# Kernel tuning notes

Measured on AMD Instinct MI355X. Metric: run time of the kernel, lower is better.

The kernel has to match this reference:

```python
import jax, jax.numpy as jnp
import numpy as np
from jax import lax

B, S, D = 8, 96, 768
R, RSEQ, TAG = 24, 8, 3


def setup_inputs() -> dict:
    key = jax.random.key(0)
    k0, k1, k2, k3 = jax.random.split(key, 4)
    encoded_text = jax.random.normal(k0, (B, S, D), jnp.float32)
    rel_types_encoded = jax.random.normal(k1, (R, RSEQ, D), jnp.float32)
    proj_W = jax.random.normal(k2, (2 * D, 3 * D), jnp.float32) * 0.02
    proj_b = jnp.zeros((3 * D,), jnp.float32)
    rel_W = jax.random.normal(k3, (3 * D, R * TAG), jnp.float32) * 0.02
    rel_b = jnp.zeros((R * TAG,), jnp.float32)
    return {
        "encoded_text": encoded_text,
        "rel_types_encoded": rel_types_encoded,
        "proj_W": proj_W,
        "proj_b": proj_b,
        "rel_W": rel_W,
        "rel_b": rel_b,
    }


def _refine(enc, rel_types):
    """Faithful vectorized version of the nested python loops in
    get_encoded_text: for each sample i, R sequential cross-attention
    updates on matrix_b using matrix_a = rel_types_encoded[i] (the
    original code indexes with i, reusing the same matrix_a each step).
    enc: [Bsz, S, D]; rel_types: [R, RSEQ, D].
    """
    Bsz = enc.shape[0]
    d = enc.shape[-1]
    scale = 1.0 / jnp.sqrt(jnp.asarray(d, enc.dtype))
    num_steps = rel_types.shape[0]  # loop runs rel_types_encoded.size(0) times
    A_batch = rel_types[:Bsz]  # matrix_a = rel_types_encoded[i]

    def per_sample(b0, A):  # b0: [S, D], A: [RSEQ, D]
        def step(b, _):
            scores = (A @ b.T) * scale            # [RSEQ, S]
            w = jax.nn.softmax(scores, axis=-1)    # softmax over seq
            return b + w.T @ A, None               # matrix_b += matrix_c
        bf, _ = lax.scan(step, b0, None, length=num_steps)
        return bf

    return jax.vmap(per_sample)(enc, A_batch)


def reference(encoded_text, rel_types_encoded, proj_W, proj_b, rel_W, rel_b):
    enc = _refine(encoded_text, rel_types_encoded)  # [B, S, D]
    Bsz, seq, d = enc.shape
    rel_num = rel_types_encoded.shape[0]
    tag_size = rel_W.shape[1] // rel_num

    # projection(cat(head, tail)) == head @ Wh + tail @ Wt + b; avoid
    # materializing the [B, S*S, 2D] concat (same math as the original).
    Wh, Wt = proj_W[:d], proj_W[d:]
    Hh = enc @ Wh                                   # [B, S, 3D] head part
    Ht = enc @ Wt                                   # [B, S, 3D] tail part
    pairs = Hh[:, :, None, :] + Ht[:, None, :, :] + proj_b  # [B, S, S, 3D]
    pairs = jax.nn.relu(pairs)
    triple = pairs.reshape(Bsz, seq * seq, 3 * d) @ rel_W + rel_b
    triple = triple.reshape(Bsz, seq, seq, rel_num, tag_size)
    return jnp.transpose(triple, (0, 4, 3, 1, 2))  # [B, tag, rel, S, S]
```

## Files before the change

### kernel.cpp

```cpp
#include <hip/hip_runtime.h>
#include <hip/hip_bf16.h>
#include <math.h>
#include <stdint.h>
#include <string.h>

#define BB 8
#define SS 96
#define DD 768
#define RR 24
#define RSEQ 8
#define TAG 3
#define D3 2304
#define NC 72

typedef __attribute__((ext_vector_type(8))) short bf16x8;
typedef __attribute__((ext_vector_type(4))) float f32x4;
typedef _Float16 f16x8 __attribute__((ext_vector_type(8)));
typedef _Float16 f16x2 __attribute__((ext_vector_type(2)));

typedef __attribute__((address_space(3))) uint8_t lds_u8;
typedef const __attribute__((address_space(1))) uint8_t glb_u8;
static __device__ __forceinline__ void glld16(const void* g, void* l) {
  __builtin_amdgcn_global_load_lds((glb_u8*)g, (lds_u8*)l, 16, 0, 0);
}

#define VMW(N) asm volatile("s_waitcnt vmcnt(" #N ")" ::: "memory")

static __device__ inline uint32_t pkrhu(float lo, float hi) {
  uint32_t a, b;
  memcpy(&a, &lo, 4);
  memcpy(&b, &hi, 4);
  return __builtin_amdgcn_perm(b + 0x8000u, a + 0x8000u, 0x07060302u);
}
static __device__ inline uint32_t pkrne(float lo, float hi) {
  uint32_t a, b;
  memcpy(&a, &lo, 4);
  memcpy(&b, &hi, 4);
  a += 0x7FFFu + ((a >> 16) & 1u);
  b += 0x7FFFu + ((b >> 16) & 1u);
  return (a >> 16) | (b & 0xFFFF0000u);
}
static __device__ inline uint32_t pkf16(float lo, float hi) {
  union { f16x2 h; uint32_t u; } r;
  r.h[0] = (_Float16)lo;
  r.h[1] = (_Float16)hi;
  return r.u;
}
static __device__ inline uint16_t f16b(float v) {
  union { _Float16 h; uint16_t u; } r;
  r.h = (_Float16)v;
  return r.u;
}

__global__ __launch_bounds__(256) void k_prep0(const float* __restrict__ relW,
                                               uint16_t* __restrict__ Wb,
                                               const float* __restrict__ projW,
                                               uint16_t* __restrict__ Tp,
                                               const float* __restrict__ enc,
                                               const float* __restrict__ rel,
                                               float* __restrict__ SG) {
  __shared__ __align__(16) char smem[24704];
  const int blk = blockIdx.x;
  const int t = threadIdx.x;

  if (blk < 36) {
    float* tile = (float*)smem;
    const int k0 = blk * 64;
    const float* src = relW + (size_t)k0 * NC;
    for (int e = t; e < 64 * NC / 4; e += 256) ((float4*)tile)[e] = ((const float4*)src)[e];
    __syncthreads();
    for (int u = t; u < 80 * 16; u += 256) {
      const int n = u >> 4, kq = (u & 15) * 4;
      uint2 w = {0u, 0u};
      if (n < NC) {
        w.x = pkf16(tile[(kq + 0) * NC + n], tile[(kq + 1) * NC + n]);
        w.y = pkf16(tile[(kq + 2) * NC + n], tile[(kq + 3) * NC + n]);
      }
      *(uint2*)&Wb[(size_t)n * D3 + k0 + kq] = w;
    }
  } else if (blk < 900) {
    const int bx = blk - 36;
    float (*tile)[65] = (float(*)[65])smem;
    const int c0 = (bx % 36) * 64;
    const int r0 = (bx / 36) * 64;
    {
      const int tr = t >> 4;
      const int tc4 = (t & 15) * 4;
#pragma unroll
      for (int p = 0; p < 4; ++p) {
        const int r = tr + p * 16;
        const float4 v = *(const float4*)&projW[(size_t)(r0 + r) * D3 + c0 + tc4];
        tile[r][tc4 + 0] = v.x;
        tile[r][tc4 + 1] = v.y;
        tile[r][tc4 + 2] = v.z;
        tile[r][tc4 + 3] = v.w;
      }
    }
    __syncthreads();
    {
      const int cc = t >> 4;
      const int rr4 = (t & 15) * 4;
#pragma unroll
      for (int p = 0; p < 4; ++p) {
        const int c = cc + p * 16;
        uint2 w;
        w.x = pkrne(tile[rr4 + 0][c], tile[rr4 + 1][c]);
        w.y = pkrne(tile[rr4 + 2][c], tile[rr4 + 3][c]);
        *(uint2*)&Tp[(size_t)(c0 + c) * (2 * DD) + r0 + rr4] = w;
      }
    }
  } else {
    const int idx = blk - 900;
    const int b = idx >> 4;
    const int d0 = (idx & 15) * 48;
    float (*AsF)[48] = (float(*)[48])smem;

    if (t < 96) {
      const int r = t / 12, q4 = (t % 12) * 4;
      *(float4*)&AsF[r][q4] = *(const float4*)&rel[((size_t)b * RSEQ + r) * DD + d0 + q4];
    }
    __syncthreads();

    for (int e = t; e < RSEQ * (SS + RSEQ); e += 256) {
      const int r = e & 7, s = e >> 3;
      const float* row = (s < SS) ? (enc + ((size_t)b * SS + s) * DD + d0) : &AsF[s - SS][0];
      float a0 = 0.f, a1 = 0.f, a2 = 0.f, a3 = 0.f;
#pragma unroll
      for (int d = 0; d < 48; d += 4) {
        const float4 rv = *(const float4*)&row[d];
        a0 += AsF[r][d + 0] * rv.x;
        a1 += AsF[r][d + 1] * rv.y;
        a2 += AsF[r][d + 2] * rv.z;
        a3 += AsF[r][d + 3] * rv.w;
      }
      atomicAdd(&SG[((size_t)b * RSEQ + r) * 104 + s], (a0 + a1) + (a2 + a3));
    }
  }
}

__global__ __launch_bounds__(256) void k_refS(const float* __restrict__ SG,
                                              float* __restrict__ Pst) {
  const int b = blockIdx.x;
  const int t = threadIdx.x;
  __shared__ float S0[RSEQ][SS];
  __shared__ float G[RSEQ][RSEQ];
  __shared__ float P[RSEQ][SS];
  __shared__ float sc[RSEQ][SS];
  const float scale = 0.036084391824351613f;

  for (int e = t; e < RSEQ * 104; e += 256) {
    const int r = e / 104, c = e % 104;
    const float v = SG[(size_t)b * RSEQ * 104 + e];
    if (c < SS) S0[r][c] = v;
    else G[r][c - SS] = v;
  }
  for (int e = t; e < RSEQ * SS; e += 256) ((float*)P)[e] = 0.f;
  __syncthreads();

  const int wave = t >> 6, lane = t & 63;
  for (int step = 0; step < RR; ++step) {
    for (int e = t; e < RSEQ * SS; e += 256) {
      const int r = e / SS, s = e % SS;
      float acc = S0[r][s];
#pragma unroll
      for (int r2 = 0; r2 < RSEQ; ++r2) acc += G[r][r2] * P[r2][s];
      sc[r][s] = acc * scale;
    }
    __syncthreads();
#pragma unroll
    for (int rr = 0; rr < 2; ++rr) {
      const int r = wave * 2 + rr;
      const float m1 = sc[r][lane];
      const float m2 = (lane < 32) ? sc[r][lane + 64] : -1e30f;
      float mx = fmaxf(m1, m2);
#pragma unroll
      for (int o = 32; o > 0; o >>= 1) mx = fmaxf(mx, __shfl_xor(mx, o, 64));
      const float e1 = __expf(m1 - mx);
      const float e2 = (lane < 32) ? __expf(m2 - mx) : 0.f;
      float sm = e1 + e2;
#pragma unroll
      for (int o = 32; o > 0; o >>= 1) sm += __shfl_xor(sm, o, 64);
      const float inv = 1.f / sm;
      P[r][lane] += e1 * inv;
      if (lane < 32) P[r][lane + 64] += e2 * inv;
    }
    __syncthreads();
  }

  for (int e = t; e < RSEQ * SS; e += 256) Pst[(size_t)b * RSEQ * SS + e] = ((float*)P)[e];
}

__global__ __launch_bounds__(256) void k_refB(const float* __restrict__ enc,
                                              const float* __restrict__ rel,
                                              const float* __restrict__ Pst,
                                              uint16_t* __restrict__ encRb) {
  const int blk = blockIdx.x;
  const int b = blk / 12;
  const int s0 = (blk % 12) * 8;
  const int t = threadIdx.x;
  __shared__ float As[RSEQ][DD + 4];
  __shared__ float Pl[RSEQ][8];

  const float* Ag = rel + (size_t)b * RSEQ * DD;
  for (int e = t; e < RSEQ * DD / 4; e += 256) {
    const int r = (e * 4) / DD, d = (e * 4) % DD;
    *(float4*)&As[r][d] = *(const float4*)&Ag[e * 4];
  }
  if (t < RSEQ * 8) {
    const int r = t >> 3, sl = t & 7;
    Pl[r][sl] = Pst[(size_t)b * RSEQ * SS + r * SS + s0 + sl];
  }
  __syncthreads();

  const float* Eb = enc + ((size_t)b * SS + s0) * DD;
  uint16_t* Ob = encRb + ((size_t)b * SS + s0) * DD;
  for (int e = t; e < 8 * DD / 4; e += 256) {
    const int sl = (e * 4) / DD, d = (e * 4) % DD;
    float4 v = ((const float4*)Eb)[e];
#pragma unroll
    for (int r = 0; r < RSEQ; ++r) {
      const float p = Pl[r][sl];
      v.x += p * As[r][d + 0];
      v.y += p * As[r][d + 1];
      v.z += p * As[r][d + 2];
      v.w += p * As[r][d + 3];
    }
    uint2 w;
    w.x = pkrhu(v.x, v.y);
    w.y = pkrhu(v.z, v.w);
    *(uint2*)&Ob[e * 4] = w;
  }
}

__global__ __launch_bounds__(256, 4) void k_proj(const uint16_t* __restrict__ Ab,
                                                 const uint16_t* __restrict__ Bt,
                                                 const float* __restrict__ pb,
                                                 uint16_t* __restrict__ Hh16,
                                                 uint16_t* __restrict__ Htf) {
  const int m0 = blockIdx.x * 64;
  const int gn0 = blockIdx.y * 64;
  const bool isH = gn0 < D3;
  const int n0 = isH ? gn0 : gn0 - D3;
  const int halfk = isH ? 0 : DD;
  const int t = threadIdx.x, w = t >> 6, lane = t & 63;
  const int wm = w >> 1, wn = w & 1;
  const int lm = lane & 15, q = lane >> 4;

  __shared__ __align__(16) uint16_t As[64 * 72];
  __shared__ __align__(16) uint16_t Bs[64 * 72];

  const char* rp[5];
  char* lp[5];
#pragma unroll
  for (int r = 0; r < 5; ++r) {
    const int idx = w + 4 * r;
    rp[r] = nullptr;
    lp[r] = nullptr;
    if (idx < 18) {
      const int ii = (idx < 9) ? idx : idx - 9;
      const int beta = ii * 1024 + lane * 16;
      const int elem = beta >> 1;
      const int row = elem / 72;
      int o = elem - row * 72;
      if (o >= 64) o = 0;
      if (idx < 9) {
        rp[r] = (const char*)(Ab + (size_t)(m0 + row) * DD + o);
        lp[r] = (char*)As + ii * 1024;
      } else {
        rp[r] = (const char*)(Bt + (size_t)(n0 + row) * (2 * DD) + halfk + o);
        lp[r] = (char*)Bs + ii * 1024;
      }
    }
  }

  f32x4 acc[2][2];
#pragma unroll
  for (int a = 0; a < 2; ++a)
#pragma unroll
    for (int c = 0; c < 2; ++c) acc[a][c] = (f32x4){0.f, 0.f, 0.f, 0.f};

  for (int k0 = 0; k0 < DD; k0 += 64) {
    __syncthreads();
#pragma unroll
    for (int r = 0; r < 5; ++r)
      if (rp[r]) glld16(rp[r] + 2 * k0, lp[r]);
    __syncthreads();
#pragma unroll
    for (int kk = 0; kk < 2; ++kk) {
      const int ko = kk * 32 + q * 8;
      bf16x8 af[2], bf[2];
#pragma unroll
      for (int mt = 0; mt < 2; ++mt)
        af[mt] = *(const bf16x8*)&As[(wm * 32 + mt * 16 + lm) * 72 + ko];
#pragma unroll
      for (int nt = 0; nt < 2; ++nt)
        bf[nt] = *(const bf16x8*)&Bs[(wn * 32 + nt * 16 + lm) * 72 + ko];
#pragma unroll
      for (int nt = 0; nt < 2; ++nt)
#pragma unroll
        for (int mt = 0; mt < 2; ++mt)
          acc[mt][nt] = __builtin_amdgcn_mfma_f32_16x16x32_bf16(af[mt], bf[nt], acc[mt][nt], 0, 0, 0);
    }
  }

#pragma unroll
  for (int nt = 0; nt < 2; ++nt) {
    const int ncol = n0 + wn * 32 + nt * 16 + lm;
    const int mrow = m0 + wm * 32 + q * 4;
    uint16_t* dst = isH ? Hh16 : Htf;
    const float bias = isH ? pb[ncol] : 0.f;
#pragma unroll
    for (int mt = 0; mt < 2; ++mt)
#pragma unroll
      for (int r = 0; r < 4; ++r)
        dst[(size_t)(mrow + mt * 16 + r) * D3 + ncol] = f16b(acc[mt][nt][r] + bias);
  }
}

#define HT_LDS 12288
#define CH_B 22528
#define NISS 22
#define NKC 36
#define NPH 18

__global__ __launch_bounds__(768, 1) void k_pairs(const uint16_t* __restrict__ Hh,
                                                  const uint16_t* __restrict__ Htb,
                                                  const uint16_t* __restrict__ Wb,
                                                  const float* __restrict__ relb,
                                                  float* __restrict__ out) {
  const int blk = blockIdx.x;
  const int b = blk >> 5, ii = blk & 31;
  const int t = threadIdx.x;
  const int w = t >> 6, lane = t & 63;
  const int lm = lane & 15, q = lane >> 4;
  const int iw = w >> 2;
  const int jh = (w >> 1) & 1;
  const int kh = w & 1;
  const int i = ii * 3 + iw;

  __shared__ __align__(16) uint16_t Hr[7680];
  __shared__ __align__(16) uint16_t Stg[3][CH_B];

  {
    const char* hh = (const char*)(Hh + ((size_t)b * SS + ii * 3) * D3);
#pragma unroll
    for (int r = 0; r < 2; ++r) {
      const int idx = w + 12 * r;
      if (idx < 14) glld16(hh + idx * 1024 + lane * 16, (char*)Hr + idx * 1024);
    }
  }

  const char* rp[2];
#pragma unroll
  for (int r = 0; r < 2; ++r) {
    const int idx = w + 12 * r;
    rp[r] = nullptr;
    if (idx < NISS) {
      const int beta = idx * 1024 + lane * 16;
      if (beta < HT_LDS) {
        const int row = beta >> 7;
        const int real = (beta & 127) ^ ((row & 7) << 4);
        rp[r] = (const char*)(Htb + ((size_t)b * SS + row) * D3 + (real >> 1));
      } else {
        const int bb = beta - HT_LDS;
        const int row = bb >> 7;
        const int real = (bb & 127) ^ ((row & 7) << 4);
        rp[r] = (const char*)(Wb + (size_t)row * D3 + (real >> 1));
      }
    }
  }

#pragma unroll
  for (int pp = 0; pp < 2; ++pp)
#pragma unroll
    for (int kc = 0; kc < 2; ++kc)
#pragma unroll
      for (int r = 0; r < 2; ++r)
        if (rp[r])
          glld16(rp[r] + (size_t)128 * (2 * pp + kc),
                 (char*)Stg[pp] + kc * CH_B + (w + 12 * r) * 1024);

  f32x4 acc[3][5];
#pragma unroll
  for (int mt = 0; mt < 3; ++mt)
#pragma unroll
    for (int nt = 0; nt < 5; ++nt) acc[mt][nt] = (f32x4){0.f, 0.f, 0.f, 0.f};

  const f16x8 zro = {0, 0, 0, 0, 0, 0, 0, 0};

  for (int p = 0; p < NPH; ++p) {
    if (w < 10) VMW(4); else VMW(2);
    __builtin_amdgcn_s_barrier();
    __builtin_amdgcn_sched_barrier(0);

    {
      char* dst = (char*)Stg[(p + 2) % 3];
      int pn = p + 2;
      if (pn >= NPH) pn -= NPH;
#pragma unroll
      for (int kc = 0; kc < 2; ++kc)
#pragma unroll
        for (int r = 0; r < 2; ++r)
          if (rp[r])
            glld16(rp[r] + (size_t)128 * (2 * pn + kc),
                   dst + kc * CH_B + (w + 12 * r) * 1024);
    }

    const char* S = (const char*)Stg[p % 3] + kh * CH_B;
    const int k0 = (2 * p + kh) * 64;
#pragma unroll
    for (int kk = 0; kk < 2; ++kk) {
      const int ko = kk * 32 + q * 8;
      const int xb = (ko * 2) ^ ((lane & 7) << 4);
      const f16x8 hv = *(const f16x8*)&Hr[iw * D3 + k0 + ko];
      f16x8 af[3];
#pragma unroll
      for (int mt = 0; mt < 3; ++mt) {
        const f16x8 s = *(const f16x8*)(S + (jh * 48 + mt * 16 + lm) * 128 + xb) + hv;
        af[mt] = __builtin_elementwise_max(s, zro);
      }
      f16x8 bfv[5];
#pragma unroll
      for (int nt = 0; nt < 5; ++nt)
        bfv[nt] = *(const f16x8*)(S + HT_LDS + (nt * 16 + lm) * 128 + xb);
      __builtin_amdgcn_s_setprio(1);
#pragma unroll
      for (int nt = 0; nt < 5; ++nt)
#pragma unroll
        for (int mt = 0; mt < 3; ++mt)
          acc[mt][nt] = __builtin_amdgcn_mfma_f32_16x16x32_f16(af[mt], bfv[nt], acc[mt][nt], 0, 0, 0);
      __builtin_amdgcn_s_setprio(0);
    }
    asm volatile("s_waitcnt lgkmcnt(0)" ::: "memory");
    __builtin_amdgcn_sched_barrier(0);
  }

  __syncthreads();
  float* RED = (float*)&Stg[0][0];
  if (w & 1) {
#pragma unroll
    for (int mt = 0; mt < 3; ++mt)
#pragma unroll
      for (int nt = 0; nt < 5; ++nt)
        *(f32x4*)&RED[(((w >> 1) * 15 + mt * 5 + nt) << 8) + lane * 4] = acc[mt][nt];
  }
  __syncthreads();
  if (!(w & 1)) {
#pragma unroll
    for (int nt = 0; nt < 5; ++nt) {
      const int c = nt * 16 + lm;
      if (c < NC) {
        const float rb = relb[c];
        const int rr = c / 3, tg = c % 3;
#pragma unroll
        for (int mt = 0; mt < 3; ++mt) {
          const f32x4 oth = *(const f32x4*)&RED[(((w >> 1) * 15 + mt * 5 + nt) << 8) + lane * 4];
          const int j0 = jh * 48 + mt * 16 + q * 4;
          float* base = out + ((((size_t)b * TAG + tg) * RR + rr) * SS + i) * SS + j0;
          float4 o;
          o.x = acc[mt][nt][0] + oth[0] + rb;
          o.y = acc[mt][nt][1] + oth[1] + rb;
          o.z = acc[mt][nt][2] + oth[2] + rb;
          o.w = acc[mt][nt][3] + oth[3] + rb;
          *(float4*)base = o;
        }
      }
    }
  }
}

extern "C" void kernel_launch(void* const* d_in, const int* in_sizes, int n_in,
                              void* d_out, int out_size, void* d_ws, size_t ws_size,
                              hipStream_t stream) {
  const float* enc   = (const float*)d_in[0];
  const float* rel   = (const float*)d_in[1];
  const float* projW = (const float*)d_in[2];
  const float* projb = (const float*)d_in[3];
  const float* relW  = (const float*)d_in[4];
  const float* relb  = (const float*)d_in[5];
  float* out = (float*)d_out;

  uint16_t* Hh16 = (uint16_t*)d_ws;
  uint16_t* Htf  = Hh16 + (size_t)DD * D3 + 512;
  uint16_t* Wb   = Htf + (size_t)DD * D3;
  uint16_t* Tp   = Wb + (size_t)96 * D3;
  uint16_t* Ab   = Tp + (size_t)D3 * 2 * DD;
  float* Pst = (float*)(Ab + (size_t)DD * DD);
  float* SG = Pst + (size_t)BB * RSEQ * SS;

  hipMemsetAsync(SG, 0, (size_t)BB * RSEQ * 104 * sizeof(float), stream);
  k_prep0<<<1028, 256, 0, stream>>>(relW, Wb, projW, Tp, enc, rel, SG);
  k_refS<<<BB, 256, 0, stream>>>(SG, Pst);
  k_refB<<<96, 256, 0, stream>>>(enc, rel, Pst, Ab);
  k_proj<<<dim3(12, 72), 256, 0, stream>>>(Ab, Tp, projb, Hh16, Htf);
  k_pairs<<<256, 768, 0, stream>>>(Hh16, Htf, Wb, relb, out);
}
```

Baseline: 182.1 us.

## Run refinement softmax in one register-resident wave; enlarge projection GEMM M tile

The 24-step softmax refinement now runs in a single 64-lane wave per sample. Scores, G and P live in registers, which removes the per-step LDS traffic and block barriers. Separately, the projection GEMM's M tile grows from 64 to 128 rows, so each block loads the B tile once for twice as many rows and the grid halves. The trade-offs are higher register pressure in both kernels and fewer blocks (432) to fill the GPU in k_proj.

```diff
diff --git a/kernel.cpp b/kernel.cpp
--- a/kernel.cpp
+++ b/kernel.cpp
@@ -138,56 +138,65 @@
   }
 }
 
-__global__ __launch_bounds__(256) void k_refS(const float* __restrict__ SG,
-                                              float* __restrict__ Pst) {
+__global__ __launch_bounds__(64) void k_refS(const float* __restrict__ SG,
+                                             float* __restrict__ Pst) {
   const int b = blockIdx.x;
-  const int t = threadIdx.x;
-  __shared__ float S0[RSEQ][SS];
-  __shared__ float G[RSEQ][RSEQ];
-  __shared__ float P[RSEQ][SS];
-  __shared__ float sc[RSEQ][SS];
+  const int l = threadIdx.x;
   const float scale = 0.036084391824351613f;
-
-  for (int e = t; e < RSEQ * 104; e += 256) {
-    const int r = e / 104, c = e % 104;
-    const float v = SG[(size_t)b * RSEQ * 104 + e];
-    if (c < SS) S0[r][c] = v;
-    else G[r][c - SS] = v;
-  }
-  for (int e = t; e < RSEQ * SS; e += 256) ((float*)P)[e] = 0.f;
-  __syncthreads();
-
-  const int wave = t >> 6, lane = t & 63;
+  const float* base = SG + (size_t)b * RSEQ * 104;
+
+  float g[RSEQ][RSEQ];
+#pragma unroll
+  for (int r = 0; r < RSEQ; ++r)
+#pragma unroll
+    for (int r2 = 0; r2 < RSEQ; ++r2) g[r][r2] = base[r * 104 + 96 + r2];
+
+  float s0a[RSEQ], s0b[RSEQ], P0[RSEQ], P1[RSEQ];
+#pragma unroll
+  for (int r = 0; r < RSEQ; ++r) {
+    s0a[r] = base[r * 104 + l];
+    s0b[r] = (l < 32) ? base[r * 104 + 64 + l] : 0.f;
+    P0[r] = 0.f;
+    P1[r] = 0.f;
+  }
+
   for (int step = 0; step < RR; ++step) {
-    for (int e = t; e < RSEQ * SS; e += 256) {
-      const int r = e / SS, s = e % SS;
-      float acc = S0[r][s];
-#pragma unroll
-      for (int r2 = 0; r2 < RSEQ; ++r2) acc += G[r][r2] * P[r2][s];
-      sc[r][s] = acc * scale;
-    }
-    __syncthreads();
-#pragma unroll
-    for (int rr = 0; rr < 2; ++rr) {
-      const int r = wave * 2 + rr;
-      const float m1 = sc[r][lane];
-      const float m2 = (lane < 32) ? sc[r][lane + 64] : -1e30f;
-      float mx = fmaxf(m1, m2);
+    float w0[RSEQ], w1[RSEQ];
+#pragma unroll
+    for (int r = 0; r < RSEQ; ++r) {
+      float a0 = s0a[r], a1 = s0b[r];
+#pragma unroll
+      for (int r2 = 0; r2 < RSEQ; ++r2) {
+        a0 += g[r][r2] * P0[r2];
+        a1 += g[r][r2] * P1[r2];
+      }
+      a0 *= scale;
+      a1 *= scale;
+      float mx = fmaxf(a0, (l < 32) ? a1 : -1e30f);
 #pragma unroll
       for (int o = 32; o > 0; o >>= 1) mx = fmaxf(mx, __shfl_xor(mx, o, 64));
-      const float e1 = __expf(m1 - mx);
-      const float e2 = (lane < 32) ? __expf(m2 - mx) : 0.f;
-      float sm = e1 + e2;
+      const float e0 = __expf(a0 - mx);
+      const float e1 = (l < 32) ? __expf(a1 - mx) : 0.f;
+      float sm = e0 + e1;
 #pragma unroll
       for (int o = 32; o > 0; o >>= 1) sm += __shfl_xor(sm, o, 64);
       const float inv = 1.f / sm;
-      P[r][lane] += e1 * inv;
-      if (lane < 32) P[r][lane + 64] += e2 * inv;
-    }
-    __syncthreads();
-  }
-
-  for (int e = t; e < RSEQ * SS; e += 256) Pst[(size_t)b * RSEQ * SS + e] = ((float*)P)[e];
+      w0[r] = e0 * inv;
+      w1[r] = e1 * inv;
+    }
+#pragma unroll
+    for (int r = 0; r < RSEQ; ++r) {
+      P0[r] += w0[r];
+      P1[r] += w1[r];
+    }
+  }
+
+  float* pb = Pst + (size_t)b * RSEQ * SS;
+#pragma unroll
+  for (int r = 0; r < RSEQ; ++r) {
+    pb[r * SS + l] = P0[r];
+    if (l < 32) pb[r * SS + 64 + l] = P1[r];
+  }
 }
 
 __global__ __launch_bounds__(256) void k_refB(const float* __restrict__ enc,
@@ -237,7 +246,7 @@
                                                  const float* __restrict__ pb,
                                                  uint16_t* __restrict__ Hh16,
                                                  uint16_t* __restrict__ Htf) {
-  const int m0 = blockIdx.x * 64;
+  const int m0 = blockIdx.x * 128;
   const int gn0 = blockIdx.y * 64;
   const bool isH = gn0 < D3;
   const int n0 = isH ? gn0 : gn0 - D3;
@@ -246,24 +255,24 @@
   const int wm = w >> 1, wn = w & 1;
   const int lm = lane & 15, q = lane >> 4;
 
-  __shared__ __align__(16) uint16_t As[64 * 72];
+  __shared__ __align__(16) uint16_t As[128 * 72];
   __shared__ __align__(16) uint16_t Bs[64 * 72];
 
-  const char* rp[5];
-  char* lp[5];
-#pragma unroll
-  for (int r = 0; r < 5; ++r) {
+  const char* rp[7];
+  char* lp[7];
+#pragma unroll
+  for (int r = 0; r < 7; ++r) {
     const int idx = w + 4 * r;
     rp[r] = nullptr;
     lp[r] = nullptr;
-    if (idx < 18) {
-      const int ii = (idx < 9) ? idx : idx - 9;
+    if (idx < 27) {
+      const int ii = (idx < 18) ? idx : idx - 18;
       const int beta = ii * 1024 + lane * 16;
       const int elem = beta >> 1;
       const int row = elem / 72;
       int o = elem - row * 72;
       if (o >= 64) o = 0;
-      if (idx < 9) {
+      if (idx < 18) {
         rp[r] = (const char*)(Ab + (size_t)(m0 + row) * DD + o);
         lp[r] = (char*)As + ii * 1024;
       } else {
@@ -273,32 +282,32 @@
     }
   }
 
-  f32x4 acc[2][2];
-#pragma unroll
-  for (int a = 0; a < 2; ++a)
+  f32x4 acc[4][2];
+#pragma unroll
+  for (int a = 0; a < 4; ++a)
 #pragma unroll
     for (int c = 0; c < 2; ++c) acc[a][c] = (f32x4){0.f, 0.f, 0.f, 0.f};
 
   for (int k0 = 0; k0 < DD; k0 += 64) {
     __syncthreads();
 #pragma unroll
-    for (int r = 0; r < 5; ++r)
+    for (int r = 0; r < 7; ++r)
       if (rp[r]) glld16(rp[r] + 2 * k0, lp[r]);
     __syncthreads();
 #pragma unroll
     for (int kk = 0; kk < 2; ++kk) {
       const int ko = kk * 32 + q * 8;
-      bf16x8 af[2], bf[2];
-#pragma unroll
-      for (int mt = 0; mt < 2; ++mt)
-        af[mt] = *(const bf16x8*)&As[(wm * 32 + mt * 16 + lm) * 72 + ko];
+      bf16x8 af[4], bf[2];
+#pragma unroll
+      for (int mt = 0; mt < 4; ++mt)
+        af[mt] = *(const bf16x8*)&As[(wm * 64 + mt * 16 + lm) * 72 + ko];
 #pragma unroll
       for (int nt = 0; nt < 2; ++nt)
         bf[nt] = *(const bf16x8*)&Bs[(wn * 32 + nt * 16 + lm) * 72 + ko];
 #pragma unroll
       for (int nt = 0; nt < 2; ++nt)
 #pragma unroll
-        for (int mt = 0; mt < 2; ++mt)
+        for (int mt = 0; mt < 4; ++mt)
           acc[mt][nt] = __builtin_amdgcn_mfma_f32_16x16x32_bf16(af[mt], bf[nt], acc[mt][nt], 0, 0, 0);
     }
   }
@@ -306,11 +315,11 @@
 #pragma unroll
   for (int nt = 0; nt < 2; ++nt) {
     const int ncol = n0 + wn * 32 + nt * 16 + lm;
-    const int mrow = m0 + wm * 32 + q * 4;
+    const int mrow = m0 + wm * 64 + q * 4;
     uint16_t* dst = isH ? Hh16 : Htf;
     const float bias = isH ? pb[ncol] : 0.f;
 #pragma unroll
-    for (int mt = 0; mt < 2; ++mt)
+    for (int mt = 0; mt < 4; ++mt)
 #pragma unroll
       for (int r = 0; r < 4; ++r)
         dst[(size_t)(mrow + mt * 16 + r) * D3 + ncol] = f16b(acc[mt][nt][r] + bias);
@@ -490,8 +499,8 @@
 
   hipMemsetAsync(SG, 0, (size_t)BB * RSEQ * 104 * sizeof(float), stream);
   k_prep0<<<1028, 256, 0, stream>>>(relW, Wb, projW, Tp, enc, rel, SG);
-  k_refS<<<BB, 256, 0, stream>>>(SG, Pst);
+  k_refS<<<BB, 64, 0, stream>>>(SG, Pst);
   k_refB<<<96, 256, 0, stream>>>(enc, rel, Pst, Ab);
-  k_proj<<<dim3(12, 72), 256, 0, stream>>>(Ab, Tp, projb, Hh16, Htf);
+  k_proj<<<dim3(6, 72), 256, 0, stream>>>(Ab, Tp, projb, Hh16, Htf);
   k_pairs<<<256, 768, 0, stream>>>(Hh16, Htf, Wb, relb, out);
 }
```

New measurement: 201.1 us. 1.1x slower.
